# Optimization experiments

Hardware: AMD Instinct MI355X
Metric: run time of the kernel (lower is better)

## Reference

```python
import jax, jax.numpy as jnp
import numpy as np

N, M = 30000, 32
VX, VY, VZ = 0.2, 0.2, 4.0
XOFF, YOFF, ZOFF = 0.1, -39.9, -1.0  # vx/2+pc_range[0], vy/2+pc_range[1], vz/2+pc_range[2]
EPS = 1e-3
H = 3  # num_heads, head_dim = 3 // 3 = 1


def setup_inputs() -> dict:
    key = jax.random.key(0)
    ks = jax.random.split(key, 13)
    features = jax.random.normal(ks[0], (N, M, 4), jnp.float32)
    num_points = jax.random.randint(ks[1], (N,), 1, M + 1, dtype=jnp.int32)
    coors = jax.random.randint(ks[2], (N, 4), 0, 352, dtype=jnp.int32)
    # PFN layer params (Linear 10->64 no bias, BN1d affine)
    pfn_w = jax.random.normal(ks[3], (10, 64), jnp.float32) * 0.1
    bn_gamma = jnp.ones((64,), jnp.float32)
    bn_beta = jnp.zeros((64,), jnp.float32)
    # PillarAttention: MHA on 3-dim coords, 3 heads of dim 1
    wq = jax.random.normal(ks[4], (3, 3), jnp.float32) * 0.5
    wk = jax.random.normal(ks[5], (3, 3), jnp.float32) * 0.5
    wv = jax.random.normal(ks[6], (3, 3), jnp.float32) * 0.5
    wo = jax.random.normal(ks[7], (3, 3), jnp.float32) * 0.5
    bq = jax.random.normal(ks[8], (3,), jnp.float32) * 0.02
    bk = jax.random.normal(ks[9], (3,), jnp.float32) * 0.02
    bv = jax.random.normal(ks[10], (3,), jnp.float32) * 0.02
    bo = jax.random.normal(ks[11], (3,), jnp.float32) * 0.02
    return dict(features=features, num_points=num_points, coors=coors,
                pfn_w=pfn_w, bn_gamma=bn_gamma, bn_beta=bn_beta,
                wq=wq, wk=wk, wv=wv, wo=wo, bq=bq, bk=bk, bv=bv, bo=bo)


def _pillar_attention(xyz, wq, wk, wv, wo, bq, bk, bv, bo):
    # xyz: (N, M, 3); 3 heads of dim 1 -> per-head score is an outer product
    q = xyz @ wq + bq  # (N, M, 3)
    k = xyz @ wk + bk
    v = xyz @ wv + bv
    # head_dim = 1 => scale = 1/sqrt(1) = 1
    scores = jnp.einsum('nih,njh->nhij', q, k)          # (N, H, M, M)
    attn = jax.nn.softmax(scores, axis=-1)
    out = jnp.einsum('nhij,njh->nih', attn, v)          # (N, M, 3)
    return out @ wo + bo


def reference(features, num_points, coors, pfn_w, bn_gamma, bn_beta,
              wq, wk, wv, wo, bq, bk, bv, bo):
    dtype = features.dtype
    xyz = features[:, :, :3]  # original coords (attn & cluster use these, pre in-place write)

    # PillarAttention on raw xyz, then max over feature dim
    feat_attn = _pillar_attention(xyz, wq, wk, wv, wo, bq, bk, bv, bo)  # (N, M, 3)
    max_attn = jnp.max(feat_attn, axis=-1, keepdims=True)              # (N, M, 1)

    npts = num_points.astype(dtype)[:, None, None]                      # (N,1,1)
    # cluster center offsets (uses original xyz)
    points_mean = jnp.sum(xyz, axis=1, keepdims=True) / npts
    f_cluster = xyz - points_mean                                       # (N, M, 3)

    # voxel center offsets; coors = [batch, z, y, x]
    cf = coors.astype(dtype)
    cx = cf[:, 3] * VX + XOFF
    cy = cf[:, 2] * VY + YOFF
    cz = cf[:, 1] * VZ + ZOFF
    f_center = jnp.stack([xyz[:, :, 0] - cx[:, None],
                          xyz[:, :, 1] - cy[:, None],
                          xyz[:, :, 2] - cz[:, None]], axis=-1)          # (N, M, 3)

    # legacy=True in-place bug: features[:, :, :3] becomes f_center before concat
    feats = jnp.concatenate([f_center, features[:, :, 3:], f_cluster, f_center], axis=-1)  # (N, M, 10)

    # mask out padded points
    mask = (jnp.arange(M)[None, :] < num_points[:, None]).astype(dtype)[:, :, None]
    feats = feats * mask

    # PFNLayer (last_vfe=True): Linear -> BN1d (train-mode stats over N*M) -> LeakyReLU
    x = feats @ pfn_w                                                    # (N, M, 64)
    mean = jnp.mean(x, axis=(0, 1))
    var = jnp.var(x, axis=(0, 1))
    x = (x - mean) * jax.lax.rsqrt(var + EPS) * bn_gamma + bn_beta
    x = jax.nn.leaky_relu(x, negative_slope=0.01)                        # (N, M, 64)

    # attention-weighted max pool fused with plain max pool
    fa = max_attn * x / jnp.sum(max_attn, axis=1, keepdims=True)
    fa = jnp.max(fa, axis=1, keepdims=True)                              # (N, 1, 64)
    fm = jnp.max(x, axis=1, keepdims=True)                               # (N, 1, 64)
    f = (fa + fm) * 0.5
    return f[:, 0, :]                                                    # (N, 64)
```

## Files before the change

kernel.cpp:

```cpp
#include <hip/hip_runtime.h>
#include <float.h>
#include <math.h>

constexpr int NP = 30000;
constexpr int M  = 32;
constexpr float VXc = 0.2f, VYc = 0.2f, VZc = 4.0f;
constexpr float XOFFc = 0.1f, YOFFc = -39.9f, ZOFFc = -1.0f;

typedef __attribute__((ext_vector_type(8)))  short bf16x8;
typedef __attribute__((ext_vector_type(16))) float f32x16;

#define WAVE_LDS_FENCE() asm volatile("s_waitcnt lgkmcnt(0)" ::: "memory")

__device__ __forceinline__ unsigned short f2bf(float x) {
    unsigned int u = __builtin_bit_cast(unsigned int, x);
    u = (u + 0x7fffu + ((u >> 16) & 1u)) >> 16;
    return (unsigned short)u;
}

__global__ __launch_bounds__(256) void stats_kernel(
    const float4* __restrict__ fp,
    const int*    __restrict__ num_points,
    const int*    __restrict__ coors,
    float*        __restrict__ Sp)
{
    float S[35];
#pragma unroll
    for (int k = 0; k < 35; ++k) S[k] = 0.f;

    const int stride = gridDim.x * blockDim.x;

    for (int p = blockIdx.x * blockDim.x + threadIdx.x; p < NP * M; p += stride) {
        const int n = p >> 5;
        const int i = p & 31;
        const float4 f = fp[p];

        float sx = f.x, sy = f.y, sz = f.z;
#pragma unroll
        for (int m = 16; m >= 1; m >>= 1) {
            sx += __shfl_xor(sx, m, 32);
            sy += __shfl_xor(sy, m, 32);
            sz += __shfl_xor(sz, m, 32);
        }
        const int npts = num_points[n];
        const float inv = __builtin_amdgcn_rcpf((float)npts);
        const int c1 = coors[4 * n + 1], c2 = coors[4 * n + 2], c3 = coors[4 * n + 3];
        const float cx = (float)c3 * VXc + XOFFc;
        const float cy = (float)c2 * VYc + YOFFc;
        const float cz = (float)c1 * VZc + ZOFFc;
        const bool valid = (i < npts);

        float u[7];
        u[0] = valid ? f.x - cx : 0.f;
        u[1] = valid ? f.y - cy : 0.f;
        u[2] = valid ? f.z - cz : 0.f;
        u[3] = valid ? f.w      : 0.f;
        u[4] = valid ? f.x - sx * inv : 0.f;
        u[5] = valid ? f.y - sy * inv : 0.f;
        u[6] = valid ? f.z - sz * inv : 0.f;

#pragma unroll
        for (int k = 0; k < 7; ++k) S[k] += u[k];
        int idx = 7;
#pragma unroll
        for (int k = 0; k < 7; ++k)
#pragma unroll
            for (int l = k; l < 7; ++l)
                S[idx++] += u[k] * u[l];
    }

#pragma unroll
    for (int k = 0; k < 35; ++k) {
#pragma unroll
        for (int m = 32; m >= 1; m >>= 1) S[k] += __shfl_xor(S[k], m, 64);
    }

    __shared__ float part[4][35];
    const int wid = threadIdx.x >> 6, ln = threadIdx.x & 63;
    if (ln == 0) {
#pragma unroll
        for (int k = 0; k < 35; ++k) part[wid][k] = S[k];
    }
    __syncthreads();
    if (threadIdx.x < 35) {
        Sp[blockIdx.x * 35 + threadIdx.x] =
            part[0][threadIdx.x] + part[1][threadIdx.x] +
            part[2][threadIdx.x] + part[3][threadIdx.x];
    }
}

__global__ __launch_bounds__(320) void affine_kernel(
    const float* __restrict__ Sp,
    int nsb,
    const float* __restrict__ pfn_w,
    const float* __restrict__ gamma,
    const float* __restrict__ beta,
    unsigned short* __restrict__ Wpk)
{
    __shared__ double sh[8][36];
    __shared__ double Sd[35];
    __shared__ float a_sh[64], b_sh[64];
    const int tid = threadIdx.x;

    if (tid < 280) {
        const int k = tid % 35;
        const int c = tid / 35;
        double acc = 0.0;
        for (int b = c; b < nsb; b += 8)
            acc += (double)Sp[b * 35 + k];
        sh[c][k] = acc;
    }
    __syncthreads();
    if (tid < 35) {
        double a = 0.0;
#pragma unroll
        for (int c = 0; c < 8; ++c) a += sh[c][tid];
        Sd[tid] = a;
    }
    __syncthreads();

    if (tid < 64) {
        const int c = tid;
        double w7[7];
        w7[0] = (double)pfn_w[0 * 64 + c] + (double)pfn_w[7 * 64 + c];
        w7[1] = (double)pfn_w[1 * 64 + c] + (double)pfn_w[8 * 64 + c];
        w7[2] = (double)pfn_w[2 * 64 + c] + (double)pfn_w[9 * 64 + c];
        w7[3] = (double)pfn_w[3 * 64 + c];
        w7[4] = (double)pfn_w[4 * 64 + c];
        w7[5] = (double)pfn_w[5 * 64 + c];
        w7[6] = (double)pfn_w[6 * 64 + c];

        const double invNM = 1.0 / ((double)NP * (double)M);
        double mean = 0.0;
#pragma unroll
        for (int k = 0; k < 7; ++k) mean += Sd[k] * w7[k];
        mean *= invNM;

        double ex2 = 0.0;
        int idx = 7;
#pragma unroll
        for (int k = 0; k < 7; ++k)
#pragma unroll
            for (int l = k; l < 7; ++l) {
                double t = Sd[idx++] * w7[k] * w7[l];
                ex2 += (k == l) ? t : 2.0 * t;
            }
        ex2 *= invNM;

        double var = ex2 - mean * mean;
        double a = (double)gamma[c] / sqrt(var + 1e-3);
        a_sh[c] = (float)a;
        b_sh[c] = (float)((double)beta[c] - mean * a);
    }
    __syncthreads();

    if (tid < 256) {
        const int s = tid;
        const int v = s >> 7;
        const int t = (s >> 6) & 1;
        const int l = s & 63;
        const int half = l >> 5;
        const int n = (l & 31) + 32 * t;
        unsigned short val[8] = {0, 0, 0, 0, 0, 0, 0, 0};
        if (half == v) {
            const float a = a_sh[n];
            float w7[7];
            w7[0] = pfn_w[0 * 64 + n] + pfn_w[7 * 64 + n];
            w7[1] = pfn_w[1 * 64 + n] + pfn_w[8 * 64 + n];
            w7[2] = pfn_w[2 * 64 + n] + pfn_w[9 * 64 + n];
            w7[3] = pfn_w[3 * 64 + n];
            w7[4] = pfn_w[4 * 64 + n];
            w7[5] = pfn_w[5 * 64 + n];
            w7[6] = pfn_w[6 * 64 + n];
#pragma unroll
            for (int j = 0; j < 7; ++j) val[j] = f2bf(w7[j] * a);
            val[7] = f2bf(b_sh[n]);
        }
#pragma unroll
        for (int j = 0; j < 8; ++j) Wpk[s * 8 + j] = val[j];
    }
}

__global__ __launch_bounds__(256) void main_kernel(
    const float4* __restrict__ fp,
    const int*    __restrict__ num_points,
    const int*    __restrict__ coors,
    const unsigned short* __restrict__ Wpk,
    const float*  __restrict__ wq, const float* __restrict__ wk,
    const float*  __restrict__ wv, const float* __restrict__ wo,
    const float*  __restrict__ bq, const float* __restrict__ bk,
    const float*  __restrict__ bv, const float* __restrict__ bo,
    float*        __restrict__ out)
{
    const int tid  = threadIdx.x;
    const int w    = tid >> 6;
    const int lane = tid & 63;
    const int half = lane >> 5;
    const int i    = lane & 31;
    const int pair = blockIdx.x * 4 + w;
    const int n    = pair * 2 + half;

    __shared__ float kv_s[4][2][32][8];
    __shared__ float r_s[4][2][32];

    const float4 f = fp[(size_t)n * M + i];
    const int np = num_points[n];
    const int c1 = coors[4 * n + 1], c2 = coors[4 * n + 2], c3 = coors[4 * n + 3];
    const bf16x8 bfA0 = *reinterpret_cast<const bf16x8*>(Wpk + (size_t)(  0 + lane) * 8);
    const bf16x8 bfA1 = *reinterpret_cast<const bf16x8*>(Wpk + (size_t)( 64 + lane) * 8);
    const bf16x8 bfB0 = *reinterpret_cast<const bf16x8*>(Wpk + (size_t)(128 + lane) * 8);
    const bf16x8 bfB1 = *reinterpret_cast<const bf16x8*>(Wpk + (size_t)(192 + lane) * 8);

    float q[3], kk[3], vv[3];
#pragma unroll
    for (int h = 0; h < 3; ++h) {
        q[h]  = f.x * wq[0 * 3 + h] + f.y * wq[1 * 3 + h] + f.z * wq[2 * 3 + h] + bq[h];
        kk[h] = f.x * wk[0 * 3 + h] + f.y * wk[1 * 3 + h] + f.z * wk[2 * 3 + h] + bk[h];
        vv[h] = f.x * wv[0 * 3 + h] + f.y * wv[1 * 3 + h] + f.z * wv[2 * 3 + h] + bv[h];
    }
    *reinterpret_cast<float4*>(&kv_s[w][half][i][0]) = make_float4(kk[0], vv[0], kk[1], vv[1]);
    *reinterpret_cast<float2*>(&kv_s[w][half][i][4]) = make_float2(kk[2], vv[2]);

    float sx = f.x, sy = f.y, sz = f.z;
#pragma unroll
    for (int m = 16; m >= 1; m >>= 1) {
        sx += __shfl_xor(sx, m, 32);
        sy += __shfl_xor(sy, m, 32);
        sz += __shfl_xor(sz, m, 32);
    }
    WAVE_LDS_FENCE();

    const float LOG2E = 1.4426950408889634f;
    float qh2[3];
#pragma unroll
    for (int h = 0; h < 3; ++h) qh2[h] = q[h] * LOG2E;

    float den[3] = {0.f, 0.f, 0.f}, num[3] = {0.f, 0.f, 0.f};
#pragma unroll
    for (int j = 0; j < 32; ++j) {
        const float4 kv01 = *reinterpret_cast<const float4*>(&kv_s[w][half][j][0]);
        const float2 kv2  = *reinterpret_cast<const float2*>(&kv_s[w][half][j][4]);
        float e0 = __builtin_amdgcn_exp2f(qh2[0] * kv01.x);
        float e1 = __builtin_amdgcn_exp2f(qh2[1] * kv01.z);
        float e2 = __builtin_amdgcn_exp2f(qh2[2] * kv2.x);
        den[0] += e0; num[0] = __builtin_fmaf(e0, kv01.y, num[0]);
        den[1] += e1; num[1] = __builtin_fmaf(e1, kv01.w, num[1]);
        den[2] += e2; num[2] = __builtin_fmaf(e2, kv2.y,  num[2]);
    }
    const float o0 = num[0] * __builtin_amdgcn_rcpf(den[0]);
    const float o1 = num[1] * __builtin_amdgcn_rcpf(den[1]);
    const float o2 = num[2] * __builtin_amdgcn_rcpf(den[2]);

    float fa0 = o0 * wo[0] + o1 * wo[3] + o2 * wo[6] + bo[0];
    float fa1 = o0 * wo[1] + o1 * wo[4] + o2 * wo[7] + bo[1];
    float fa2 = o0 * wo[2] + o1 * wo[5] + o2 * wo[8] + bo[2];
    float ma  = fmaxf(fa0, fmaxf(fa1, fa2));

    float sum_ma = ma;
#pragma unroll
    for (int m = 16; m >= 1; m >>= 1) sum_ma += __shfl_xor(sum_ma, m, 32);
    r_s[w][half][i] = ma * __builtin_amdgcn_rcpf(sum_ma);

    const float inv = __builtin_amdgcn_rcpf((float)np);
    const float cx = (float)c3 * VXc + XOFFc;
    const float cy = (float)c2 * VYc + YOFFc;
    const float cz = (float)c1 * VZc + ZOFFc;
    const bool valid = (i < np);

    float u[7];
    u[0] = valid ? f.x - cx : 0.f;
    u[1] = valid ? f.y - cy : 0.f;
    u[2] = valid ? f.z - cz : 0.f;
    u[3] = valid ? f.w      : 0.f;
    u[4] = valid ? f.x - sx * inv : 0.f;
    u[5] = valid ? f.y - sy * inv : 0.f;
    u[6] = valid ? f.z - sz * inv : 0.f;

    unsigned int w32[4];
    w32[0] = (unsigned int)f2bf(u[0]) | ((unsigned int)f2bf(u[1]) << 16);
    w32[1] = (unsigned int)f2bf(u[2]) | ((unsigned int)f2bf(u[3]) << 16);
    w32[2] = (unsigned int)f2bf(u[4]) | ((unsigned int)f2bf(u[5]) << 16);
    w32[3] = (unsigned int)f2bf(u[6]) | (0x3F80u << 16);

    union { unsigned int wd[4]; bf16x8 v; } ua, ub;
#pragma unroll
    for (int e = 0; e < 4; ++e) {
        ua.wd[e] = (half == 0) ? w32[e] : 0u;
        ub.wd[e] = (half == 1) ? w32[e] : 0u;
    }

    f32x16 accA0 = {}, accA1 = {}, accB0 = {}, accB1 = {};
    accA0 = __builtin_amdgcn_mfma_f32_32x32x16_bf16(ua.v, bfA0, accA0, 0, 0, 0);
    accA1 = __builtin_amdgcn_mfma_f32_32x32x16_bf16(ua.v, bfA1, accA1, 0, 0, 0);
    accB0 = __builtin_amdgcn_mfma_f32_32x32x16_bf16(ub.v, bfB0, accB0, 0, 0, 0);
    accB1 = __builtin_amdgcn_mfma_f32_32x32x16_bf16(ub.v, bfB1, accB1, 0, 0, 0);

    WAVE_LDS_FENCE();

    {
        float4 rg4[4];
#pragma unroll
        for (int g = 0; g < 4; ++g)
            rg4[g] = *reinterpret_cast<const float4*>(&r_s[w][0][g * 8 + 4 * half]);

        float fm0 = -FLT_MAX, fv0 = -FLT_MAX, fm1 = -FLT_MAX, fv1 = -FLT_MAX;
#pragma unroll
        for (int rg = 0; rg < 16; ++rg) {
            const float rr = rg4[rg >> 2][rg & 3];
            float y0 = accA0[rg];
            y0 = fmaxf(y0, 0.01f * y0);
            fm0 = fmaxf(fm0, y0); fv0 = fmaxf(fv0, rr * y0);
            float y1 = accA1[rg];
            y1 = fmaxf(y1, 0.01f * y1);
            fm1 = fmaxf(fm1, y1); fv1 = fmaxf(fv1, rr * y1);
        }
        fm0 = fmaxf(fm0, __shfl_xor(fm0, 32, 64));
        fv0 = fmaxf(fv0, __shfl_xor(fv0, 32, 64));
        fm1 = fmaxf(fm1, __shfl_xor(fm1, 32, 64));
        fv1 = fmaxf(fv1, __shfl_xor(fv1, 32, 64));
        const float res = (half == 0) ? 0.5f * (fv0 + fm0) : 0.5f * (fv1 + fm1);
        out[(size_t)(pair * 2) * 64 + 32 * half + i] = res;
    }

    {
        float4 rg4[4];
#pragma unroll
        for (int g = 0; g < 4; ++g)
            rg4[g] = *reinterpret_cast<const float4*>(&r_s[w][1][g * 8 + 4 * half]);

        float fm0 = -FLT_MAX, fv0 = -FLT_MAX, fm1 = -FLT_MAX, fv1 = -FLT_MAX;
#pragma unroll
        for (int rg = 0; rg < 16; ++rg) {
            const float rr = rg4[rg >> 2][rg & 3];
            float y0 = accB0[rg];
            y0 = fmaxf(y0, 0.01f * y0);
            fm0 = fmaxf(fm0, y0); fv0 = fmaxf(fv0, rr * y0);
            float y1 = accB1[rg];
            y1 = fmaxf(y1, 0.01f * y1);
            fm1 = fmaxf(fm1, y1); fv1 = fmaxf(fv1, rr * y1);
        }
        fm0 = fmaxf(fm0, __shfl_xor(fm0, 32, 64));
        fv0 = fmaxf(fv0, __shfl_xor(fv0, 32, 64));
        fm1 = fmaxf(fm1, __shfl_xor(fm1, 32, 64));
        fv1 = fmaxf(fv1, __shfl_xor(fv1, 32, 64));
        const float res = (half == 0) ? 0.5f * (fv0 + fm0) : 0.5f * (fv1 + fm1);
        out[(size_t)(pair * 2 + 1) * 64 + 32 * half + i] = res;
    }
}

extern "C" void kernel_launch(void* const* d_in, const int* in_sizes, int n_in,
                              void* d_out, int out_size, void* d_ws, size_t ws_size,
                              hipStream_t stream) {
    const float4* feats  = (const float4*)d_in[0];
    const int*    npts   = (const int*)d_in[1];
    const int*    coors  = (const int*)d_in[2];
    const float*  pfn_w  = (const float*)d_in[3];
    const float*  gamma  = (const float*)d_in[4];
    const float*  beta   = (const float*)d_in[5];
    const float*  wq     = (const float*)d_in[6];
    const float*  wk     = (const float*)d_in[7];
    const float*  wv     = (const float*)d_in[8];
    const float*  wo     = (const float*)d_in[9];
    const float*  bq     = (const float*)d_in[10];
    const float*  bk     = (const float*)d_in[11];
    const float*  bv     = (const float*)d_in[12];
    const float*  bo     = (const float*)d_in[13];
    float*        out    = (float*)d_out;

    int nsb = 480;
    if (ws_size > 0 && ws_size < (size_t)(480 * 140 + 8192)) {
        size_t avail = ws_size > 8192 ? ws_size - 8192 : 140;
        int fit = (int)(avail / 140);
        nsb = fit < 1 ? 1 : (fit > 480 ? 480 : fit);
    }
    size_t wpk_off = ((size_t)(nsb * 140) + 255) & ~(size_t)255;
    float*          Sp  = (float*)d_ws;
    unsigned short* Wpk = (unsigned short*)((char*)d_ws + wpk_off);

    stats_kernel<<<nsb, 256, 0, stream>>>(feats, npts, coors, Sp);
    affine_kernel<<<1, 320, 0, stream>>>(Sp, nsb, pfn_w, gamma, beta, Wpk);
    main_kernel<<<NP / 8, 256, 0, stream>>>(feats, npts, coors, Wpk,
                                            wq, wk, wv, wo, bq, bk, bv, bo, out);
}
```

Before: 145.3 us.

## Process four pillars per wave with prefetch of next pillar pair

Each wave now loops over two pillar pairs instead of one, and the grid is halved to match. While the current pair is being computed, the loop issues the global loads for the next pair's features, num_points and coors. The bf16 weight fragments are loaded once per wave and reused across both pairs. The aim is to hide global-load latency and amortize per-wave setup, at the cost of half as many waves in flight and a few more registers held for the prefetched data.

```diff
diff --git a/kernel.cpp b/kernel.cpp
--- a/kernel.cpp
+++ b/kernel.cpp
@@ -197,154 +197,174 @@
     const int lane = tid & 63;
     const int half = lane >> 5;
     const int i    = lane & 31;
-    const int pair = blockIdx.x * 4 + w;
-    const int n    = pair * 2 + half;
+    const int wave = blockIdx.x * 4 + w;
+    const int nb   = wave * 4;
 
     __shared__ float kv_s[4][2][32][8];
     __shared__ float r_s[4][2][32];
 
-    const float4 f = fp[(size_t)n * M + i];
-    const int np = num_points[n];
-    const int c1 = coors[4 * n + 1], c2 = coors[4 * n + 2], c3 = coors[4 * n + 3];
     const bf16x8 bfA0 = *reinterpret_cast<const bf16x8*>(Wpk + (size_t)(  0 + lane) * 8);
     const bf16x8 bfA1 = *reinterpret_cast<const bf16x8*>(Wpk + (size_t)( 64 + lane) * 8);
     const bf16x8 bfB0 = *reinterpret_cast<const bf16x8*>(Wpk + (size_t)(128 + lane) * 8);
     const bf16x8 bfB1 = *reinterpret_cast<const bf16x8*>(Wpk + (size_t)(192 + lane) * 8);
 
-    float q[3], kk[3], vv[3];
-#pragma unroll
-    for (int h = 0; h < 3; ++h) {
-        q[h]  = f.x * wq[0 * 3 + h] + f.y * wq[1 * 3 + h] + f.z * wq[2 * 3 + h] + bq[h];
-        kk[h] = f.x * wk[0 * 3 + h] + f.y * wk[1 * 3 + h] + f.z * wk[2 * 3 + h] + bk[h];
-        vv[h] = f.x * wv[0 * 3 + h] + f.y * wv[1 * 3 + h] + f.z * wv[2 * 3 + h] + bv[h];
-    }
-    *reinterpret_cast<float4*>(&kv_s[w][half][i][0]) = make_float4(kk[0], vv[0], kk[1], vv[1]);
-    *reinterpret_cast<float2*>(&kv_s[w][half][i][4]) = make_float2(kk[2], vv[2]);
-
-    float sx = f.x, sy = f.y, sz = f.z;
-#pragma unroll
-    for (int m = 16; m >= 1; m >>= 1) {
-        sx += __shfl_xor(sx, m, 32);
-        sy += __shfl_xor(sy, m, 32);
-        sz += __shfl_xor(sz, m, 32);
-    }
-    WAVE_LDS_FENCE();
+    float4 f = fp[(size_t)(nb + half) * M + i];
+    int np = num_points[nb + half];
+    int c1 = coors[4 * (nb + half) + 1];
+    int c2 = coors[4 * (nb + half) + 2];
+    int c3 = coors[4 * (nb + half) + 3];
 
     const float LOG2E = 1.4426950408889634f;
-    float qh2[3];
-#pragma unroll
-    for (int h = 0; h < 3; ++h) qh2[h] = q[h] * LOG2E;
-
-    float den[3] = {0.f, 0.f, 0.f}, num[3] = {0.f, 0.f, 0.f};
-#pragma unroll
-    for (int j = 0; j < 32; ++j) {
-        const float4 kv01 = *reinterpret_cast<const float4*>(&kv_s[w][half][j][0]);
-        const float2 kv2  = *reinterpret_cast<const float2*>(&kv_s[w][half][j][4]);
-        float e0 = __builtin_amdgcn_exp2f(qh2[0] * kv01.x);
-        float e1 = __builtin_amdgcn_exp2f(qh2[1] * kv01.z);
-        float e2 = __builtin_amdgcn_exp2f(qh2[2] * kv2.x);
-        den[0] += e0; num[0] = __builtin_fmaf(e0, kv01.y, num[0]);
-        den[1] += e1; num[1] = __builtin_fmaf(e1, kv01.w, num[1]);
-        den[2] += e2; num[2] = __builtin_fmaf(e2, kv2.y,  num[2]);
-    }
-    const float o0 = num[0] * __builtin_amdgcn_rcpf(den[0]);
-    const float o1 = num[1] * __builtin_amdgcn_rcpf(den[1]);
-    const float o2 = num[2] * __builtin_amdgcn_rcpf(den[2]);
-
-    float fa0 = o0 * wo[0] + o1 * wo[3] + o2 * wo[6] + bo[0];
-    float fa1 = o0 * wo[1] + o1 * wo[4] + o2 * wo[7] + bo[1];
-    float fa2 = o0 * wo[2] + o1 * wo[5] + o2 * wo[8] + bo[2];
-    float ma  = fmaxf(fa0, fmaxf(fa1, fa2));
-
-    float sum_ma = ma;
-#pragma unroll
-    for (int m = 16; m >= 1; m >>= 1) sum_ma += __shfl_xor(sum_ma, m, 32);
-    r_s[w][half][i] = ma * __builtin_amdgcn_rcpf(sum_ma);
-
-    const float inv = __builtin_amdgcn_rcpf((float)np);
-    const float cx = (float)c3 * VXc + XOFFc;
-    const float cy = (float)c2 * VYc + YOFFc;
-    const float cz = (float)c1 * VZc + ZOFFc;
-    const bool valid = (i < np);
-
-    float u[7];
-    u[0] = valid ? f.x - cx : 0.f;
-    u[1] = valid ? f.y - cy : 0.f;
-    u[2] = valid ? f.z - cz : 0.f;
-    u[3] = valid ? f.w      : 0.f;
-    u[4] = valid ? f.x - sx * inv : 0.f;
-    u[5] = valid ? f.y - sy * inv : 0.f;
-    u[6] = valid ? f.z - sz * inv : 0.f;
-
-    unsigned int w32[4];
-    w32[0] = (unsigned int)f2bf(u[0]) | ((unsigned int)f2bf(u[1]) << 16);
-    w32[1] = (unsigned int)f2bf(u[2]) | ((unsigned int)f2bf(u[3]) << 16);
-    w32[2] = (unsigned int)f2bf(u[4]) | ((unsigned int)f2bf(u[5]) << 16);
-    w32[3] = (unsigned int)f2bf(u[6]) | (0x3F80u << 16);
-
-    union { unsigned int wd[4]; bf16x8 v; } ua, ub;
-#pragma unroll
-    for (int e = 0; e < 4; ++e) {
-        ua.wd[e] = (half == 0) ? w32[e] : 0u;
-        ub.wd[e] = (half == 1) ? w32[e] : 0u;
-    }
-
-    f32x16 accA0 = {}, accA1 = {}, accB0 = {}, accB1 = {};
-    accA0 = __builtin_amdgcn_mfma_f32_32x32x16_bf16(ua.v, bfA0, accA0, 0, 0, 0);
-    accA1 = __builtin_amdgcn_mfma_f32_32x32x16_bf16(ua.v, bfA1, accA1, 0, 0, 0);
-    accB0 = __builtin_amdgcn_mfma_f32_32x32x16_bf16(ub.v, bfB0, accB0, 0, 0, 0);
-    accB1 = __builtin_amdgcn_mfma_f32_32x32x16_bf16(ub.v, bfB1, accB1, 0, 0, 0);
-
-    WAVE_LDS_FENCE();
-
-    {
-        float4 rg4[4];
-#pragma unroll
-        for (int g = 0; g < 4; ++g)
-            rg4[g] = *reinterpret_cast<const float4*>(&r_s[w][0][g * 8 + 4 * half]);
-
-        float fm0 = -FLT_MAX, fv0 = -FLT_MAX, fm1 = -FLT_MAX, fv1 = -FLT_MAX;
-#pragma unroll
-        for (int rg = 0; rg < 16; ++rg) {
-            const float rr = rg4[rg >> 2][rg & 3];
-            float y0 = accA0[rg];
-            y0 = fmaxf(y0, 0.01f * y0);
-            fm0 = fmaxf(fm0, y0); fv0 = fmaxf(fv0, rr * y0);
-            float y1 = accA1[rg];
-            y1 = fmaxf(y1, 0.01f * y1);
-            fm1 = fmaxf(fm1, y1); fv1 = fmaxf(fv1, rr * y1);
-        }
-        fm0 = fmaxf(fm0, __shfl_xor(fm0, 32, 64));
-        fv0 = fmaxf(fv0, __shfl_xor(fv0, 32, 64));
-        fm1 = fmaxf(fm1, __shfl_xor(fm1, 32, 64));
-        fv1 = fmaxf(fv1, __shfl_xor(fv1, 32, 64));
-        const float res = (half == 0) ? 0.5f * (fv0 + fm0) : 0.5f * (fv1 + fm1);
-        out[(size_t)(pair * 2) * 64 + 32 * half + i] = res;
-    }
-
-    {
-        float4 rg4[4];
-#pragma unroll
-        for (int g = 0; g < 4; ++g)
-            rg4[g] = *reinterpret_cast<const float4*>(&r_s[w][1][g * 8 + 4 * half]);
-
-        float fm0 = -FLT_MAX, fv0 = -FLT_MAX, fm1 = -FLT_MAX, fv1 = -FLT_MAX;
-#pragma unroll
-        for (int rg = 0; rg < 16; ++rg) {
-            const float rr = rg4[rg >> 2][rg & 3];
-            float y0 = accB0[rg];
-            y0 = fmaxf(y0, 0.01f * y0);
-            fm0 = fmaxf(fm0, y0); fv0 = fmaxf(fv0, rr * y0);
-            float y1 = accB1[rg];
-            y1 = fmaxf(y1, 0.01f * y1);
-            fm1 = fmaxf(fm1, y1); fv1 = fmaxf(fv1, rr * y1);
-        }
-        fm0 = fmaxf(fm0, __shfl_xor(fm0, 32, 64));
-        fv0 = fmaxf(fv0, __shfl_xor(fv0, 32, 64));
-        fm1 = fmaxf(fm1, __shfl_xor(fm1, 32, 64));
-        fv1 = fmaxf(fv1, __shfl_xor(fv1, 32, 64));
-        const float res = (half == 0) ? 0.5f * (fv0 + fm0) : 0.5f * (fv1 + fm1);
-        out[(size_t)(pair * 2 + 1) * 64 + 32 * half + i] = res;
+
+    for (int g = 0; g < 2; ++g) {
+        const int n = nb + 2 * g + half;
+
+        float4 fn = f; int npn = np, c1n = c1, c2n = c2, c3n = c3;
+        if (g < 1) {
+            const int nn = n + 2;
+            fn  = fp[(size_t)nn * M + i];
+            npn = num_points[nn];
+            c1n = coors[4 * nn + 1];
+            c2n = coors[4 * nn + 2];
+            c3n = coors[4 * nn + 3];
+        }
+
+        float q[3], kk[3], vv[3];
+#pragma unroll
+        for (int h = 0; h < 3; ++h) {
+            q[h]  = f.x * wq[0 * 3 + h] + f.y * wq[1 * 3 + h] + f.z * wq[2 * 3 + h] + bq[h];
+            kk[h] = f.x * wk[0 * 3 + h] + f.y * wk[1 * 3 + h] + f.z * wk[2 * 3 + h] + bk[h];
+            vv[h] = f.x * wv[0 * 3 + h] + f.y * wv[1 * 3 + h] + f.z * wv[2 * 3 + h] + bv[h];
+        }
+        *reinterpret_cast<float4*>(&kv_s[w][half][i][0]) = make_float4(kk[0], vv[0], kk[1], vv[1]);
+        *reinterpret_cast<float2*>(&kv_s[w][half][i][4]) = make_float2(kk[2], vv[2]);
+
+        float sx = f.x, sy = f.y, sz = f.z;
+#pragma unroll
+        for (int m = 16; m >= 1; m >>= 1) {
+            sx += __shfl_xor(sx, m, 32);
+            sy += __shfl_xor(sy, m, 32);
+            sz += __shfl_xor(sz, m, 32);
+        }
+        WAVE_LDS_FENCE();
+
+        float qh2[3];
+#pragma unroll
+        for (int h = 0; h < 3; ++h) qh2[h] = q[h] * LOG2E;
+
+        float den[3] = {0.f, 0.f, 0.f}, num[3] = {0.f, 0.f, 0.f};
+#pragma unroll
+        for (int j = 0; j < 32; ++j) {
+            const float4 kv01 = *reinterpret_cast<const float4*>(&kv_s[w][half][j][0]);
+            const float2 kv2  = *reinterpret_cast<const float2*>(&kv_s[w][half][j][4]);
+            float e0 = __builtin_amdgcn_exp2f(qh2[0] * kv01.x);
+            float e1 = __builtin_amdgcn_exp2f(qh2[1] * kv01.z);
+            float e2 = __builtin_amdgcn_exp2f(qh2[2] * kv2.x);
+            den[0] += e0; num[0] = __builtin_fmaf(e0, kv01.y, num[0]);
+            den[1] += e1; num[1] = __builtin_fmaf(e1, kv01.w, num[1]);
+            den[2] += e2; num[2] = __builtin_fmaf(e2, kv2.y,  num[2]);
+        }
+        const float o0 = num[0] * __builtin_amdgcn_rcpf(den[0]);
+        const float o1 = num[1] * __builtin_amdgcn_rcpf(den[1]);
+        const float o2 = num[2] * __builtin_amdgcn_rcpf(den[2]);
+
+        float fa0 = o0 * wo[0] + o1 * wo[3] + o2 * wo[6] + bo[0];
+        float fa1 = o0 * wo[1] + o1 * wo[4] + o2 * wo[7] + bo[1];
+        float fa2 = o0 * wo[2] + o1 * wo[5] + o2 * wo[8] + bo[2];
+        float ma  = fmaxf(fa0, fmaxf(fa1, fa2));
+
+        float sum_ma = ma;
+#pragma unroll
+        for (int m = 16; m >= 1; m >>= 1) sum_ma += __shfl_xor(sum_ma, m, 32);
+        r_s[w][half][i] = ma * __builtin_amdgcn_rcpf(sum_ma);
+
+        const float inv = __builtin_amdgcn_rcpf((float)np);
+        const float cx = (float)c3 * VXc + XOFFc;
+        const float cy = (float)c2 * VYc + YOFFc;
+        const float cz = (float)c1 * VZc + ZOFFc;
+        const bool valid = (i < np);
+
+        float u[7];
+        u[0] = valid ? f.x - cx : 0.f;
+        u[1] = valid ? f.y - cy : 0.f;
+        u[2] = valid ? f.z - cz : 0.f;
+        u[3] = valid ? f.w      : 0.f;
+        u[4] = valid ? f.x - sx * inv : 0.f;
+        u[5] = valid ? f.y - sy * inv : 0.f;
+        u[6] = valid ? f.z - sz * inv : 0.f;
+
+        unsigned int w32[4];
+        w32[0] = (unsigned int)f2bf(u[0]) | ((unsigned int)f2bf(u[1]) << 16);
+        w32[1] = (unsigned int)f2bf(u[2]) | ((unsigned int)f2bf(u[3]) << 16);
+        w32[2] = (unsigned int)f2bf(u[4]) | ((unsigned int)f2bf(u[5]) << 16);
+        w32[3] = (unsigned int)f2bf(u[6]) | (0x3F80u << 16);
+
+        union { unsigned int wd[4]; bf16x8 v; } ua, ub;
+#pragma unroll
+        for (int e = 0; e < 4; ++e) {
+            ua.wd[e] = (half == 0) ? w32[e] : 0u;
+            ub.wd[e] = (half == 1) ? w32[e] : 0u;
+        }
+
+        f32x16 accA0 = {}, accA1 = {}, accB0 = {}, accB1 = {};
+        accA0 = __builtin_amdgcn_mfma_f32_32x32x16_bf16(ua.v, bfA0, accA0, 0, 0, 0);
+        accA1 = __builtin_amdgcn_mfma_f32_32x32x16_bf16(ua.v, bfA1, accA1, 0, 0, 0);
+        accB0 = __builtin_amdgcn_mfma_f32_32x32x16_bf16(ub.v, bfB0, accB0, 0, 0, 0);
+        accB1 = __builtin_amdgcn_mfma_f32_32x32x16_bf16(ub.v, bfB1, accB1, 0, 0, 0);
+
+        WAVE_LDS_FENCE();
+
+        {
+            float4 rg4[4];
+#pragma unroll
+            for (int gg = 0; gg < 4; ++gg)
+                rg4[gg] = *reinterpret_cast<const float4*>(&r_s[w][0][gg * 8 + 4 * half]);
+
+            float fm0 = -FLT_MAX, fv0 = -FLT_MAX, fm1 = -FLT_MAX, fv1 = -FLT_MAX;
+#pragma unroll
+            for (int rg = 0; rg < 16; ++rg) {
+                const float rr = rg4[rg >> 2][rg & 3];
+                float y0 = accA0[rg];
+                y0 = fmaxf(y0, 0.01f * y0);
+                fm0 = fmaxf(fm0, y0); fv0 = fmaxf(fv0, rr * y0);
+                float y1 = accA1[rg];
+                y1 = fmaxf(y1, 0.01f * y1);
+                fm1 = fmaxf(fm1, y1); fv1 = fmaxf(fv1, rr * y1);
+            }
+            fm0 = fmaxf(fm0, __shfl_xor(fm0, 32, 64));
+            fv0 = fmaxf(fv0, __shfl_xor(fv0, 32, 64));
+            fm1 = fmaxf(fm1, __shfl_xor(fm1, 32, 64));
+            fv1 = fmaxf(fv1, __shfl_xor(fv1, 32, 64));
+            const float res = (half == 0) ? 0.5f * (fv0 + fm0) : 0.5f * (fv1 + fm1);
+            out[(size_t)(nb + 2 * g) * 64 + 32 * half + i] = res;
+        }
+
+        {
+            float4 rg4[4];
+#pragma unroll
+            for (int gg = 0; gg < 4; ++gg)
+                rg4[gg] = *reinterpret_cast<const float4*>(&r_s[w][1][gg * 8 + 4 * half]);
+
+            float fm0 = -FLT_MAX, fv0 = -FLT_MAX, fm1 = -FLT_MAX, fv1 = -FLT_MAX;
+#pragma unroll
+            for (int rg = 0; rg < 16; ++rg) {
+                const float rr = rg4[rg >> 2][rg & 3];
+                float y0 = accB0[rg];
+                y0 = fmaxf(y0, 0.01f * y0);
+                fm0 = fmaxf(fm0, y0); fv0 = fmaxf(fv0, rr * y0);
+                float y1 = accB1[rg];
+                y1 = fmaxf(y1, 0.01f * y1);
+                fm1 = fmaxf(fm1, y1); fv1 = fmaxf(fv1, rr * y1);
+            }
+            fm0 = fmaxf(fm0, __shfl_xor(fm0, 32, 64));
+            fv0 = fmaxf(fv0, __shfl_xor(fv0, 32, 64));
+            fm1 = fmaxf(fm1, __shfl_xor(fm1, 32, 64));
+            fv1 = fmaxf(fv1, __shfl_xor(fv1, 32, 64));
+            const float res = (half == 0) ? 0.5f * (fv0 + fm0) : 0.5f * (fv1 + fm1);
+            out[(size_t)(nb + 2 * g + 1) * 64 + 32 * half + i] = res;
+        }
+
+        f = fn; np = npn; c1 = c1n; c2 = c2n; c3 = c3n;
     }
 }
 
@@ -379,6 +399,6 @@
 
     stats_kernel<<<nsb, 256, 0, stream>>>(feats, npts, coors, Sp);
     affine_kernel<<<1, 320, 0, stream>>>(Sp, nsb, pfn_w, gamma, beta, Wpk);
-    main_kernel<<<NP / 8, 256, 0, stream>>>(feats, npts, coors, Wpk,
-                                            wq, wk, wv, wo, bq, bk, bv, bo, out);
+    main_kernel<<<NP / 16, 256, 0, stream>>>(feats, npts, coors, Wpk,
+                                             wq, wk, wv, wo, bq, bk, bv, bo, out);
 }
```

After: 149.1 us. +2.6%, slower.
